# Optimization experiments

Hardware: AMD Instinct MI355X
Metric: run time of the kernel (lower is better)

Reference implementation:

```python
import jax, jax.numpy as jnp
import numpy as np

N = 100000
F_IN = 128
HID = 16
C = 16
E = 3200000


def setup_inputs() -> dict:
    key = jax.random.key(0)
    k1, k2, k3, k4, k5, k6 = jax.random.split(key, 6)
    x = jax.random.normal(k1, (N, F_IN), dtype=jnp.float32)
    edge_index = jax.random.randint(k2, (2, E), 0, N, dtype=jnp.int64)
    # GCNConv weight (glorot) + bias
    W1 = jax.random.normal(k3, (F_IN, HID), dtype=jnp.float32) * (1.0 / np.sqrt(F_IN))
    b1 = jnp.zeros((HID,), dtype=jnp.float32)
    # pooling linear
    Wp = jax.random.normal(k4, (HID, C), dtype=jnp.float32) * (1.0 / np.sqrt(HID))
    bp = jax.random.normal(k5, (C,), dtype=jnp.float32) * 0.01
    return {"x": x, "W1": W1, "b1": b1, "Wp": Wp, "bp": bp, "edge_index": edge_index}


def gcn_conv(x, W, b, edge_index, num_nodes):
    # PyG GCNConv: add self-loops, symmetric normalization D^-1/2 (A+I) D^-1/2
    loop = jnp.arange(num_nodes, dtype=edge_index.dtype)
    src = jnp.concatenate([edge_index[0], loop])
    dst = jnp.concatenate([edge_index[1], loop])
    ones = jnp.ones_like(dst, dtype=x.dtype)
    deg = jax.ops.segment_sum(ones, dst, num_segments=num_nodes)  # [N]
    dinv = jnp.where(deg > 0, jax.lax.rsqrt(deg), 0.0)
    norm = dinv[src] * dinv[dst]  # [E+N]
    h = x @ W  # [N, HID] transform before aggregation (fewer bytes moved)
    msgs = h[src] * norm[:, None]  # gather + scale
    agg = jax.ops.segment_sum(msgs, dst, num_segments=num_nodes)  # scatter-add
    return agg + b


def reference(x, W1, b1, Wp, bp, edge_index):
    h = jax.nn.relu(gcn_conv(x, W1, b1, edge_index, N))  # [N, HID]
    s = jax.nn.softmax(h @ Wp + bp, axis=1)  # [N, C]
    return s
```

## Files before the change

### kernel.cpp

```cpp
#include <hip/hip_runtime.h>


#define PCHUNK 4096
#define SPLITS 4
#define ACH 2048

__device__ __forceinline__ float bf2f(unsigned int u16) {
    return __uint_as_float(u16 << 16);
}
__device__ __forceinline__ unsigned short f2bf(float f) {
    unsigned int u = __float_as_uint(f);
    u += 0x7fffu + ((u >> 16) & 1u);
    return (unsigned short)(u >> 16);
}

__device__ __forceinline__ void atomAddF(float* p, float v) {
    unsafeAtomicAdd(p, v);
}

__global__ __launch_bounds__(256) void k_detect(const unsigned int* __restrict__ xw,
                                                const unsigned int* __restrict__ eiw,
                                                int* __restrict__ flags,
                                                int* __restrict__ cursor) {
    __shared__ int votes[2];
    int tid = threadIdx.x;
    cursor[tid] = 0; cursor[tid + 256] = 0;
    if (tid == 0) { votes[0] = 0; votes[1] = 0; }
    __syncthreads();
    unsigned int w = xw[tid];
    unsigned int lo = w & 0xffffu;
    unsigned int elo = (lo >> 7) & 0xffu;
    int bfvote = (lo == 0u || (elo >= 100u && elo <= 140u)) ? 1 : 0;
    int nzvote = (eiw[2 * tid + 1] != 0u) ? 1 : 0;
    atomicAdd(&votes[0], bfvote);
    atomicAdd(&votes[1], nzvote);
    __syncthreads();
    if (tid == 0) {
        flags[0] = (votes[0] >= 160) ? 1 : 0;
        flags[1] = (votes[1] == 0) ? 1 : 0;
    }
}

__global__ __launch_bounds__(256) void k_part(const int* __restrict__ ei,
                                              const int* __restrict__ flags,
                                              int* __restrict__ cursor,
                                              unsigned int* __restrict__ bkt,
                                              int E, int Nn, int NB, int cap) {
    __shared__ int lhist[512];
    __shared__ int lexcl[512];
    __shared__ int lbase[512];
    __shared__ int sa[512], sb[512];
    __shared__ unsigned int stage[PCHUNK];
    __shared__ ushort sbk[PCHUNK];
    __shared__ int stot_s;
    int tid = threadIdx.x;
    lhist[tid] = 0; lhist[tid + 256] = 0;
    __syncthreads();
    int is64 = flags[1];
    int e0 = blockIdx.x * PCHUNK;
    int ss[16], dd[16];
    #pragma unroll
    for (int i = 0; i < 16; ++i) {
        int e = e0 + i * 256 + tid;
        int s = -1, d = -1;
        if (e < E) {
            if (is64) { s = ei[2 * e]; d = ei[2 * (E + e)]; }
            else      { s = ei[e];     d = ei[E + e]; }
            if ((unsigned)s >= (unsigned)Nn || (unsigned)d >= (unsigned)Nn) { s = -1; d = -1; }
        }
        ss[i] = s; dd[i] = d;
        if (d >= 0) atomicAdd(&lhist[d >> 8], 1);
    }
    __syncthreads();
    sa[tid] = lhist[tid]; sa[tid + 256] = lhist[tid + 256];
    __syncthreads();
    int* cur = sa; int* nxt = sb;
    for (int off = 1; off < 512; off <<= 1) {
        nxt[tid] = cur[tid] + ((tid >= off) ? cur[tid - off] : 0);
        int t2 = tid + 256;
        nxt[t2] = cur[t2] + ((t2 >= off) ? cur[t2 - off] : 0);
        __syncthreads();
        int* t = cur; cur = nxt; nxt = t;
    }
    lexcl[tid] = cur[tid] - lhist[tid];
    lexcl[tid + 256] = cur[tid + 256] - lhist[tid + 256];
    if (tid == 0) stot_s = cur[511];
    __syncthreads();
    for (int b = tid; b < 512; b += 256) {
        int c = lhist[b];
        if (b < NB && c > 0) {
            int base = atomicAdd(&cursor[b], c);
            lbase[b] = b * cap + base - lexcl[b];
        } else lbase[b] = 0;
        lhist[b] = lexcl[b];
    }
    __syncthreads();
    #pragma unroll
    for (int i = 0; i < 16; ++i) {
        if (dd[i] >= 0) {
            int b = dd[i] >> 8;
            int q = atomicAdd(&lhist[b], 1);
            stage[q] = (unsigned)ss[i] | ((unsigned)(dd[i] & 255) << 17);
            sbk[q] = (ushort)b;
        }
    }
    __syncthreads();
    int stot = stot_s;
    for (int q = tid; q < stot; q += 256) {
        int b = sbk[q];
        int pos = lbase[b] + q;
        if (pos < (b + 1) * cap) bkt[pos] = stage[q];
    }
}

__global__ __launch_bounds__(256) void k_gemmD(const void* __restrict__ xraw,
                                               const void* __restrict__ w1raw,
                                               const int* __restrict__ flags,
                                               const unsigned int* __restrict__ bkt,
                                               const int* __restrict__ cursor,
                                               float* __restrict__ dinv,
                                               float* __restrict__ hs,
                                               float* __restrict__ agg,
                                               int Nn, int cap) {
    __shared__ float sWt[16 * 132];
    __shared__ int ldeg[256];
    __shared__ float sdv[256];
    const int isbf = flags[0];
    const ushort* xb = (const ushort*)xraw;
    const float* xf = (const float*)xraw;
    int tid = threadIdx.x, b = blockIdx.x;
    ldeg[tid] = 0;
    if (isbf) {
        const ushort* w1 = (const ushort*)w1raw;
        for (int i = tid; i < 2048; i += 256) {
            int k = i >> 4, j = i & 15;
            sWt[j * 132 + k] = bf2f(w1[i]);
        }
    } else {
        const float* w1 = (const float*)w1raw;
        for (int i = tid; i < 2048; i += 256) {
            int k = i >> 4, j = i & 15;
            sWt[j * 132 + k] = w1[i];
        }
    }
    __syncthreads();
    int len = min(cursor[b], cap);
    int bb = b * cap;
    for (int e = tid; e < len; e += 256)
        atomicAdd(&ldeg[(bkt[bb + e] >> 17) & 255u], 1);
    __syncthreads();
    {
        float dv = rsqrtf((float)(ldeg[tid] + 1));
        sdv[tid] = dv;
        int n = (b << 8) + tid;
        if (n < Nn) dinv[n] = dv;
    }
    __syncthreads();
    int hq = tid & 3;
    int nodeq = tid >> 2;
    int n0 = (b << 8) + nodeq * 4;
    float acc[4][4] = {};
    for (int ko = 0; ko < 16; ++ko) {
        float xv[4][8];
        #pragma unroll
        for (int r = 0; r < 4; ++r) {
            int n = n0 + r;
            if (n < Nn) {
                if (isbf) {
                    uint4 q = *reinterpret_cast<const uint4*>(xb + (size_t)n * 128 + ko * 8);
                    xv[r][0] = bf2f(q.x & 0xffffu); xv[r][1] = bf2f(q.x >> 16);
                    xv[r][2] = bf2f(q.y & 0xffffu); xv[r][3] = bf2f(q.y >> 16);
                    xv[r][4] = bf2f(q.z & 0xffffu); xv[r][5] = bf2f(q.z >> 16);
                    xv[r][6] = bf2f(q.w & 0xffffu); xv[r][7] = bf2f(q.w >> 16);
                } else {
                    const float4* p = reinterpret_cast<const float4*>(xf + (size_t)n * 128 + ko * 8);
                    float4 a = p[0], bf = p[1];
                    xv[r][0] = a.x; xv[r][1] = a.y; xv[r][2] = a.z; xv[r][3] = a.w;
                    xv[r][4] = bf.x; xv[r][5] = bf.y; xv[r][6] = bf.z; xv[r][7] = bf.w;
                }
            } else {
                #pragma unroll
                for (int u = 0; u < 8; ++u) xv[r][u] = 0.f;
            }
        }
        #pragma unroll
        for (int c = 0; c < 4; ++c) {
            const float* wr = &sWt[(hq * 4 + c) * 132 + ko * 8];
            float4 w0 = *reinterpret_cast<const float4*>(wr);
            float4 w1v = *reinterpret_cast<const float4*>(wr + 4);
            #pragma unroll
            for (int r = 0; r < 4; ++r) {
                acc[r][c] += xv[r][0] * w0.x + xv[r][1] * w0.y + xv[r][2] * w0.z + xv[r][3] * w0.w
                           + xv[r][4] * w1v.x + xv[r][5] * w1v.y + xv[r][6] * w1v.z + xv[r][7] * w1v.w;
            }
        }
    }
    #pragma unroll
    for (int r = 0; r < 4; ++r) {
        int n = n0 + r;
        if (n < Nn) {
            float dv = sdv[nodeq * 4 + r];
            float4 o = make_float4(acc[r][0] * dv, acc[r][1] * dv, acc[r][2] * dv, acc[r][3] * dv);
            *reinterpret_cast<float4*>(hs + (size_t)n * 16 + hq * 4) = o;
            *reinterpret_cast<float4*>(agg + (size_t)n * 16 + hq * 4) = o;
        }
    }
}

__global__ __launch_bounds__(256) void k_aggS(const unsigned int* __restrict__ bkt,
                                              const int* __restrict__ cursor,
                                              const float* __restrict__ hs,
                                              float* __restrict__ agg, int Nn, int cap) {
    __shared__ float sAgg[4096];
    __shared__ unsigned int sSorted[ACH];
    __shared__ int cnt[256], excl[256];
    __shared__ int sc[2][256];
    __shared__ int tot_s;
    int tid = threadIdx.x;
    int b = blockIdx.x >> 2, sp = blockIdx.x & 3;
    for (int i = tid; i < 4096; i += 256) sAgg[i] = 0.f;
    int len = min(cursor[b], cap);
    int bb = b * cap;
    int s0 = (int)(((long long)len * sp) >> 2);
    int s1 = (int)(((long long)len * (sp + 1)) >> 2);
    int g = tid >> 4, j = tid & 15;
    for (int c0 = s0; c0 < s1; c0 += ACH) {
        cnt[tid] = 0;
        __syncthreads();
        unsigned ue[8];
        #pragma unroll
        for (int i = 0; i < 8; ++i) {
            int idx = c0 + i * 256 + tid;
            if (idx < s1) {
                ue[i] = bkt[bb + idx];
                atomicAdd(&cnt[(ue[i] >> 17) & 255u], 1);
            } else ue[i] = 0xffffffffu;
        }
        __syncthreads();
        int v = cnt[tid];
        sc[0][tid] = v;
        __syncthreads();
        int pi = 0;
        for (int off = 1; off < 256; off <<= 1) {
            sc[pi ^ 1][tid] = sc[pi][tid] + ((tid >= off) ? sc[pi][tid - off] : 0);
            __syncthreads();
            pi ^= 1;
        }
        int ex = sc[pi][tid] - v;
        excl[tid] = ex;
        cnt[tid] = ex;
        if (tid == 255) tot_s = sc[pi][255];
        __syncthreads();
        #pragma unroll
        for (int i = 0; i < 8; ++i) {
            if (ue[i] != 0xffffffffu) {
                int q = atomicAdd(&cnt[(ue[i] >> 17) & 255u], 1);
                sSorted[q] = ue[i];
            }
        }
        __syncthreads();
        int segS = excl[g * 16];
        int segE = (g == 15) ? tot_s : excl[g * 16 + 16];
        float acc = 0.f; int curn = -1;
        for (int k = segS; k < segE; k += 16) {
            int m = segE - k;
            unsigned e[16]; float vv[16];
            #pragma unroll
            for (int i = 0; i < 16; ++i) e[i] = (i < m) ? sSorted[k + i] : 0xffffffffu;
            #pragma unroll
            for (int i = 0; i < 16; ++i)
                vv[i] = (e[i] != 0xffffffffu) ? hs[(size_t)(e[i] & 0x1ffffu) * 16 + j] : 0.f;
            #pragma unroll
            for (int i = 0; i < 16; ++i) {
                if (e[i] != 0xffffffffu) {
                    int nn = (int)((e[i] >> 17) & 255u);
                    if (nn != curn) { if (curn >= 0) sAgg[curn * 16 + j] += acc; acc = 0.f; curn = nn; }
                    acc += vv[i];
                }
            }
        }
        if (curn >= 0) sAgg[curn * 16 + j] += acc;
        __syncthreads();
    }
    int nbase = b << 8;
    for (int i = tid; i < 4096; i += 256) {
        int n = nbase + (i >> 4);
        float v = sAgg[i];
        bool nz = (n < Nn) && (v != 0.f);
        if (__any(nz)) {
            if (n < Nn) atomAddF(&agg[(size_t)n * 16 + (i & 15)], v);
        }
    }
}

__global__ __launch_bounds__(256) void k_final(const float* __restrict__ agg,
                                               const float* __restrict__ dinv,
                                               const void* __restrict__ b1raw,
                                               const void* __restrict__ wpraw,
                                               const void* __restrict__ bpraw,
                                               const int* __restrict__ flags,
                                               void* __restrict__ outraw, int Nn) {
    __shared__ float sWp[256];
    __shared__ float sA[256];
    const int isbf = flags[0];
    int tid = threadIdx.x;
    sWp[tid] = isbf ? bf2f(((const ushort*)wpraw)[tid]) : ((const float*)wpraw)[tid];
    int n0 = blockIdx.x * 16;
    int nl = tid >> 4, c = tid & 15;
    int n = n0 + nl;
    float b1v = isbf ? bf2f(((const ushort*)b1raw)[c]) : ((const float*)b1raw)[c];
    float bpv = isbf ? bf2f(((const ushort*)bpraw)[c]) : ((const float*)bpraw)[c];
    float av = (n < Nn) ? agg[(size_t)n * 16 + c] * dinv[n] : 0.f;
    sA[tid] = fmaxf(av + b1v, 0.f);
    __syncthreads();
    float acc = bpv;
    #pragma unroll
    for (int jj = 0; jj < 16; ++jj) acc += sA[nl * 16 + jj] * sWp[jj * 16 + c];
    float m = acc;
    #pragma unroll
    for (int off = 1; off < 16; off <<= 1) m = fmaxf(m, __shfl_xor(m, off, 16));
    float ev = __expf(acc - m);
    float s = ev;
    #pragma unroll
    for (int off = 1; off < 16; off <<= 1) s += __shfl_xor(s, off, 16);
    if (n < Nn) {
        float v = ev / s;
        if (isbf) ((ushort*)outraw)[(size_t)n * 16 + c] = f2bf(v);
        else      ((float*)outraw)[(size_t)n * 16 + c] = v;
    }
}

extern "C" void kernel_launch(void* const* d_in, const int* in_sizes, int n_in,
                              void* d_out, int out_size, void* d_ws, size_t ws_size,
                              hipStream_t stream) {
    const void* x  = d_in[0];
    const void* W1 = d_in[1];
    const void* b1 = d_in[2];
    const void* Wp = d_in[3];
    const void* bp = d_in[4];
    const int*  ei = (const int*)d_in[5];

    int Nn = in_sizes[0] / 128;
    int E  = in_sizes[5] / 2;
    int NB = (Nn + 255) >> 8;

    size_t Ns = (size_t)Nn;
    char* ws = (char*)d_ws;
    size_t off = 0;
    auto alloc = [&](size_t bytes) { void* p = ws + off; off += (bytes + 63) & ~(size_t)63; return p; };
    int*   flags  = (int*)alloc(64);
    float* hs     = (float*)alloc(Ns * 16 * 4);
    float* agg    = (float*)alloc(Ns * 16 * 4);
    float* dinv   = (float*)alloc(Ns * 4);
    int*   cursor = (int*)alloc(512 * 4);
    size_t remain = (ws_size > off) ? (ws_size - off) : 0;
    int cap = (int)(remain / 4 / (size_t)NB);
    int want = 12288;
    if (cap > want) cap = want;
    cap &= ~63;
    unsigned int* bkt = (unsigned int*)alloc((size_t)NB * (size_t)cap * 4);

    k_detect<<<1, 256, 0, stream>>>((const unsigned int*)x, (const unsigned int*)ei, flags, cursor);
    k_part<<<(E + PCHUNK - 1) / PCHUNK, 256, 0, stream>>>(ei, flags, cursor, bkt, E, Nn, NB, cap);
    k_gemmD<<<NB, 256, 0, stream>>>(x, W1, flags, bkt, cursor, dinv, hs, agg, Nn, cap);
    k_aggS<<<NB * SPLITS, 256, 0, stream>>>(bkt, cursor, hs, agg, Nn, cap);
    k_final<<<(Nn + 15) / 16, 256, 0, stream>>>(agg, dinv, b1, Wp, bp, flags, d_out, Nn);
}
```

Before: 250.2 us.

## Inline dtype detection into kernels and rewrite per-node aggregation loop

Removes the separate single-block detect kernel. Each kernel now votes on the input dtype itself from the first words of x or edge_index, and a memset replaces the cursor zeroing. The aggregation inner loop now walks each destination node's segment on its own and uses a tree reduction, with clamped loads in place of branchy run-length accumulation. This cuts one launch and the divergent per-edge branching, but adds redundant voting loads in every block and drops cross-node batching of gathers.

```diff
diff --git a/kernel.cpp b/kernel.cpp
--- a/kernel.cpp
+++ b/kernel.cpp
@@ -18,31 +18,18 @@
     unsafeAtomicAdd(p, v);
 }
 
-__global__ __launch_bounds__(256) void k_detect(const unsigned int* __restrict__ xw,
-                                                const unsigned int* __restrict__ eiw,
-                                                int* __restrict__ flags,
-                                                int* __restrict__ cursor) {
-    __shared__ int votes[2];
-    int tid = threadIdx.x;
-    cursor[tid] = 0; cursor[tid + 256] = 0;
-    if (tid == 0) { votes[0] = 0; votes[1] = 0; }
+__device__ __forceinline__ int voteBf16(const unsigned int* xw, int tid, int* scratch) {
+    if (tid == 0) *scratch = 0;
     __syncthreads();
     unsigned int w = xw[tid];
     unsigned int lo = w & 0xffffu;
     unsigned int elo = (lo >> 7) & 0xffu;
-    int bfvote = (lo == 0u || (elo >= 100u && elo <= 140u)) ? 1 : 0;
-    int nzvote = (eiw[2 * tid + 1] != 0u) ? 1 : 0;
-    atomicAdd(&votes[0], bfvote);
-    atomicAdd(&votes[1], nzvote);
-    __syncthreads();
-    if (tid == 0) {
-        flags[0] = (votes[0] >= 160) ? 1 : 0;
-        flags[1] = (votes[1] == 0) ? 1 : 0;
-    }
+    if (lo == 0u || (elo >= 100u && elo <= 140u)) atomicAdd(scratch, 1);
+    __syncthreads();
+    return (*scratch >= 160) ? 1 : 0;
 }
 
 __global__ __launch_bounds__(256) void k_part(const int* __restrict__ ei,
-                                              const int* __restrict__ flags,
                                               int* __restrict__ cursor,
                                               unsigned int* __restrict__ bkt,
                                               int E, int Nn, int NB, int cap) {
@@ -53,10 +40,14 @@
     __shared__ unsigned int stage[PCHUNK];
     __shared__ ushort sbk[PCHUNK];
     __shared__ int stot_s;
+    __shared__ int v64_s;
     int tid = threadIdx.x;
     lhist[tid] = 0; lhist[tid + 256] = 0;
-    __syncthreads();
-    int is64 = flags[1];
+    if (tid == 0) v64_s = 0;
+    __syncthreads();
+    if (((const unsigned int*)ei)[2 * tid + 1] != 0u) atomicAdd(&v64_s, 1);
+    __syncthreads();
+    int is64 = (v64_s == 0) ? 1 : 0;
     int e0 = blockIdx.x * PCHUNK;
     int ss[16], dd[16];
     #pragma unroll
@@ -115,7 +106,6 @@
 
 __global__ __launch_bounds__(256) void k_gemmD(const void* __restrict__ xraw,
                                                const void* __restrict__ w1raw,
-                                               const int* __restrict__ flags,
                                                const unsigned int* __restrict__ bkt,
                                                const int* __restrict__ cursor,
                                                float* __restrict__ dinv,
@@ -125,10 +115,11 @@
     __shared__ float sWt[16 * 132];
     __shared__ int ldeg[256];
     __shared__ float sdv[256];
-    const int isbf = flags[0];
+    __shared__ int vote_s;
     const ushort* xb = (const ushort*)xraw;
     const float* xf = (const float*)xraw;
     int tid = threadIdx.x, b = blockIdx.x;
+    const int isbf = voteBf16((const unsigned int*)xraw, tid, &vote_s);
     ldeg[tid] = 0;
     if (isbf) {
         const ushort* w1 = (const ushort*)w1raw;
@@ -259,27 +250,37 @@
             }
         }
         __syncthreads();
-        int segS = excl[g * 16];
-        int segE = (g == 15) ? tot_s : excl[g * 16 + 16];
-        float acc = 0.f; int curn = -1;
-        for (int k = segS; k < segE; k += 16) {
-            int m = segE - k;
-            unsigned e[16]; float vv[16];
-            #pragma unroll
-            for (int i = 0; i < 16; ++i) e[i] = (i < m) ? sSorted[k + i] : 0xffffffffu;
-            #pragma unroll
-            for (int i = 0; i < 16; ++i)
-                vv[i] = (e[i] != 0xffffffffu) ? hs[(size_t)(e[i] & 0x1ffffu) * 16 + j] : 0.f;
-            #pragma unroll
-            for (int i = 0; i < 16; ++i) {
-                if (e[i] != 0xffffffffu) {
-                    int nn = (int)((e[i] >> 17) & 255u);
-                    if (nn != curn) { if (curn >= 0) sAgg[curn * 16 + j] += acc; acc = 0.f; curn = nn; }
-                    acc += vv[i];
+        #pragma unroll 1
+        for (int nn = 0; nn < 16; ++nn) {
+            int node = g * 16 + nn;
+            int segS = excl[node];
+            int segE = (node == 255) ? tot_s : excl[node + 1];
+            float acc = 0.f;
+            #pragma unroll 1
+            for (int base = segS; base < segE; base += 16) {
+                int m = segE - base;
+                unsigned e16[16];
+                float vv[16];
+                #pragma unroll
+                for (int i = 0; i < 16; ++i) {
+                    int idx = base + i;
+                    e16[i] = sSorted[(idx < segE) ? idx : segS];
                 }
+                #pragma unroll
+                for (int i = 0; i < 16; ++i)
+                    vv[i] = hs[(size_t)(e16[i] & 0x1ffffu) * 16 + j];
+                #pragma unroll
+                for (int i = 0; i < 16; ++i)
+                    vv[i] = (i < m) ? vv[i] : 0.f;
+                #pragma unroll
+                for (int off = 8; off >= 1; off >>= 1) {
+                    #pragma unroll
+                    for (int i = 0; i < off; ++i) vv[i] += vv[i + off];
+                }
+                acc += vv[0];
             }
-        }
-        if (curn >= 0) sAgg[curn * 16 + j] += acc;
+            if (segE > segS) sAgg[node * 16 + j] += acc;
+        }
         __syncthreads();
     }
     int nbase = b << 8;
@@ -295,15 +296,16 @@
 
 __global__ __launch_bounds__(256) void k_final(const float* __restrict__ agg,
                                                const float* __restrict__ dinv,
+                                               const void* __restrict__ xraw,
                                                const void* __restrict__ b1raw,
                                                const void* __restrict__ wpraw,
                                                const void* __restrict__ bpraw,
-                                               const int* __restrict__ flags,
                                                void* __restrict__ outraw, int Nn) {
     __shared__ float sWp[256];
     __shared__ float sA[256];
-    const int isbf = flags[0];
+    __shared__ int vote_s;
     int tid = threadIdx.x;
+    const int isbf = voteBf16((const unsigned int*)xraw, tid, &vote_s);
     sWp[tid] = isbf ? bf2f(((const ushort*)wpraw)[tid]) : ((const float*)wpraw)[tid];
     int n0 = blockIdx.x * 16;
     int nl = tid >> 4, c = tid & 15;
@@ -348,7 +350,6 @@
     char* ws = (char*)d_ws;
     size_t off = 0;
     auto alloc = [&](size_t bytes) { void* p = ws + off; off += (bytes + 63) & ~(size_t)63; return p; };
-    int*   flags  = (int*)alloc(64);
     float* hs     = (float*)alloc(Ns * 16 * 4);
     float* agg    = (float*)alloc(Ns * 16 * 4);
     float* dinv   = (float*)alloc(Ns * 4);
@@ -360,9 +361,9 @@
     cap &= ~63;
     unsigned int* bkt = (unsigned int*)alloc((size_t)NB * (size_t)cap * 4);
 
-    k_detect<<<1, 256, 0, stream>>>((const unsigned int*)x, (const unsigned int*)ei, flags, cursor);
-    k_part<<<(E + PCHUNK - 1) / PCHUNK, 256, 0, stream>>>(ei, flags, cursor, bkt, E, Nn, NB, cap);
-    k_gemmD<<<NB, 256, 0, stream>>>(x, W1, flags, bkt, cursor, dinv, hs, agg, Nn, cap);
+    hipMemsetAsync(cursor, 0, 512 * 4, stream);
+    k_part<<<(E + PCHUNK - 1) / PCHUNK, 256, 0, stream>>>(ei, cursor, bkt, E, Nn, NB, cap);
+    k_gemmD<<<NB, 256, 0, stream>>>(x, W1, bkt, cursor, dinv, hs, agg, Nn, cap);
     k_aggS<<<NB * SPLITS, 256, 0, stream>>>(bkt, cursor, hs, agg, Nn, cap);
-    k_final<<<(Nn + 15) / 16, 256, 0, stream>>>(agg, dinv, b1, Wp, bp, flags, d_out, Nn);
-}
+    k_final<<<(Nn + 15) / 16, 256, 0, stream>>>(agg, dinv, x, b1, Wp, bp, d_out, Nn);
+}
```

Result: faster. 241.2 us (-3.6%).
